# Performance work log

Hardware: AMD Instinct MI355X
Metric: run time of the kernel (lower is better)

## Reference

```python
import jax, jax.numpy as jnp
import numpy as np

N_FFT = 2048
STRIDE = 512
PAD = N_FFT // 2  # center padding removed at the end
B = 4
T = 512  # number of spectrogram frames


def _make_kernels():
    n = np.arange(N_FFT)
    # ang[out_sample, freq_bin] = 2*pi*n*k/N  (create_fourier_kernels, freq_scale='no', freq_bins=n_fft)
    ang = 2.0 * np.pi * np.outer(n, n) / N_FFT
    kernel_cos = np.cos(ang).astype(np.float32)
    kernel_sin = np.sin(ang).astype(np.float32)
    # scipy.signal.get_window('hann', N, fftbins=True) -> periodic hann
    window = (0.5 - 0.5 * np.cos(2.0 * np.pi * n / N_FFT)).astype(np.float32)
    return kernel_cos, kernel_sin, window


def setup_inputs() -> dict:
    key = jax.random.key(0)
    X = jax.random.normal(key, (B, N_FFT, T, 2), dtype=jnp.float32)
    kc, ks, w = _make_kernels()
    return {
        "X": X,
        "kernel_cos": jnp.asarray(kc),
        "kernel_sin": jnp.asarray(ks),
        "window": jnp.asarray(w),
    }


def reference(X, kernel_cos, kernel_sin, window):
    # X: (B, n_fft, T, 2) complex spectrogram (onesided=False)
    b, n_fft, t, _ = X.shape
    Xr = X[..., 0]
    Xi = X[..., 1]
    # inverse DFT via dense matmul against sinusoidal kernels (conv2d in torch):
    # frames[b, n, t] = sum_f Xr[b,f,t]*cos(2pi n f/N) - Xi[b,f,t]*sin(2pi n f/N)
    frames = (jnp.einsum('bft,nf->bnt', Xr, kernel_cos)
              - jnp.einsum('bft,nf->bnt', Xi, kernel_sin))
    frames = frames * window[None, :, None] / n_fft
    # overlap-add (torch fold): out[b, t*stride + n] += frames[b, n, t]
    out_len = n_fft + STRIDE * (t - 1)
    idx = (jnp.arange(n_fft)[:, None] + STRIDE * jnp.arange(t)[None, :]).reshape(-1)
    y = jnp.zeros((b, out_len), frames.dtype).at[:, idx].add(frames.reshape(b, -1))
    # window sum-square normalization (torch_window_sumsquare)
    w_sq = jnp.broadcast_to((window * window)[:, None], (n_fft, t)).reshape(-1)
    w_sum = jnp.zeros((out_len,), window.dtype).at[idx].add(w_sq)
    nonzero = w_sum > 1e-10
    denom = jnp.where(nonzero, w_sum, jnp.ones_like(w_sum))
    y = jnp.where(nonzero[None, :], y / denom[None, :], y)
    # center=True, length=None -> trim pad_amount from both ends
    return y[:, PAD:-PAD]
```

## Files before the change

### kernel.cpp

```cpp
#include <hip/hip_runtime.h>

#define NFFT 2048
#define TT   512
#define BB   4
#define OUTL 261632

__device__ __forceinline__ int T4(int i, int sp) {
    return ((i >> 1) << 2) | ((2 * (i & 1) + sp + (i >> 1) + (i >> 3)) & 3);
}

__device__ __forceinline__ float2 cmul(float2 a, float2 w) {
    return make_float2(a.x * w.x - a.y * w.y, a.x * w.y + a.y * w.x);
}

__device__ __forceinline__ void dft8(const float2 a[8], float2 o[8]) {
    float e0r = a[0].x + a[4].x, e0i = a[0].y + a[4].y;
    float e1r = a[0].x - a[4].x, e1i = a[0].y - a[4].y;
    float e2r = a[2].x + a[6].x, e2i = a[2].y + a[6].y;
    float e3r = a[6].y - a[2].y, e3i = a[2].x - a[6].x;
    float E0r = e0r + e2r, E0i = e0i + e2i;
    float E1r = e1r + e3r, E1i = e1i + e3i;
    float E2r = e0r - e2r, E2i = e0i - e2i;
    float E3r = e1r - e3r, E3i = e1i - e3i;
    float f0r = a[1].x + a[5].x, f0i = a[1].y + a[5].y;
    float f1r = a[1].x - a[5].x, f1i = a[1].y - a[5].y;
    float f2r = a[3].x + a[7].x, f2i = a[3].y + a[7].y;
    float f3r = a[7].y - a[3].y, f3i = a[3].x - a[7].x;
    float O0r = f0r + f2r, O0i = f0i + f2i;
    float O1r = f1r + f3r, O1i = f1i + f3i;
    float O2r = f0r - f2r, O2i = f0i - f2i;
    float O3r = f1r - f3r, O3i = f1i - f3i;
    const float h = 0.70710678118654752f;
    float W1r = h * (O1r - O1i), W1i = h * (O1r + O1i);
    float W2r = -O2i,            W2i = O2r;
    float W3r = -h * (O3r + O3i), W3i = h * (O3r - O3i);
    o[0] = make_float2(E0r + O0r, E0i + O0i);
    o[1] = make_float2(E1r + W1r, E1i + W1i);
    o[2] = make_float2(E2r + W2r, E2i + W2i);
    o[3] = make_float2(E3r + W3r, E3i + W3i);
    o[4] = make_float2(E0r - O0r, E0i - O0i);
    o[5] = make_float2(E1r - W1r, E1i - W1i);
    o[6] = make_float2(E2r - W2r, E2i - W2i);
    o[7] = make_float2(E3r - W3r, E3i - W3i);
}

__device__ __forceinline__ void twpow8(float2 o[8], float2 w1) {
    float2 w2 = cmul(w1, w1);
    float2 w3 = cmul(w2, w1);
    float2 w4 = cmul(w2, w2);
    o[1] = cmul(o[1], w1);
    o[2] = cmul(o[2], w2);
    o[3] = cmul(o[3], w3);
    o[4] = cmul(o[4], w4);
    o[5] = cmul(o[5], cmul(w4, w1));
    o[6] = cmul(o[6], cmul(w4, w2));
    o[7] = cmul(o[7], cmul(w4, w3));
}

__global__ __launch_bounds__(512, 4) void istft_k(const float* __restrict__ X,
                                                  const float* __restrict__ kc,
                                                  const float* __restrict__ ks,
                                                  const float* __restrict__ win,
                                                  float* __restrict__ out) {
    __shared__ float4 tile[4096];
    __shared__ float2 tw[256];

    const int S  = blockIdx.x;
    const int L  = ((S & 7) << 6) | (S >> 3);
    const int c0 = L * 4;
    const int b  = c0 >> 9;
    const int t0 = c0 & 511;
    const int tid = threadIdx.x;

    if (tid < 256)
        tw[tid] = make_float2(kc[2048 + tid], ks[2048 + tid]);

    const float* Xb = X + ((size_t)b * 2048 * 512 + t0) * 2;
    #pragma unroll
    for (int m = 0; m < 8; m++) {
        int f  = m * 256 + (tid >> 1);
        int sp = tid & 1;
        float4 v = *reinterpret_cast<const float4*>(Xb + (size_t)f * 1024 + sp * 4);
        tile[T4(f, sp)] = v;
    }
    __syncthreads();

    const int g = tid >> 8;
    const int u = tid & 255;

    float4 a4[8];
    float2 x0[8], x1[8], o0[8], o1[8];

    #pragma unroll
    for (int l = 0; l < 8; l++) a4[l] = tile[T4(u + 256 * l, g)];
    __syncthreads();
    #pragma unroll
    for (int l = 0; l < 8; l++) {
        x0[l] = make_float2(a4[l].x, a4[l].y);
        x1[l] = make_float2(a4[l].z, a4[l].w);
    }
    dft8(x0, o0); twpow8(o0, tw[u]);
    dft8(x1, o1); twpow8(o1, tw[u]);
    #pragma unroll
    for (int k = 0; k < 8; k++)
        tile[T4(8 * u + k, g)] = make_float4(o0[k].x, o0[k].y, o1[k].x, o1[k].y);
    __syncthreads();

    #pragma unroll
    for (int l = 0; l < 8; l++) a4[l] = tile[T4(u + 256 * l, g)];
    __syncthreads();
    #pragma unroll
    for (int l = 0; l < 8; l++) {
        x0[l] = make_float2(a4[l].x, a4[l].y);
        x1[l] = make_float2(a4[l].z, a4[l].w);
    }
    dft8(x0, o0); twpow8(o0, tw[u & ~7]);
    dft8(x1, o1); twpow8(o1, tw[u & ~7]);
    {
        int base = 64 * (u >> 3) + (u & 7);
        #pragma unroll
        for (int k = 0; k < 8; k++)
            tile[T4(base + 8 * k, g)] = make_float4(o0[k].x, o0[k].y, o1[k].x, o1[k].y);
    }
    __syncthreads();

    #pragma unroll
    for (int l = 0; l < 8; l++) a4[l] = tile[T4(u + 256 * l, g)];
    __syncthreads();
    #pragma unroll
    for (int l = 0; l < 8; l++) {
        x0[l] = make_float2(a4[l].x, a4[l].y);
        x1[l] = make_float2(a4[l].z, a4[l].w);
    }
    dft8(x0, o0); twpow8(o0, tw[u & ~63]);
    dft8(x1, o1); twpow8(o1, tw[u & ~63]);
    {
        int base = 512 * (u >> 6) + (u & 63);
        #pragma unroll
        for (int k = 0; k < 8; k++)
            tile[T4(base + 64 * k, g)] = make_float4(o0[k].x, o0[k].y, o1[k].x, o1[k].y);
    }
    __syncthreads();

    #pragma unroll
    for (int half = 0; half < 2; half++) {
        int uu = u + 256 * half;
        float4 d0 = tile[T4(uu, g)];
        float4 d1 = tile[T4(uu + 512, g)];
        float4 d2 = tile[T4(uu + 1024, g)];
        float4 d3 = tile[T4(uu + 1536, g)];
        float p0 = d0.x + d2.x, p1 = d0.x - d2.x;
        float p2 = d1.x + d3.x, p3 = d3.y - d1.y;
        float q0 = d0.z + d2.z, q1 = d0.z - d2.z;
        float q2 = d1.z + d3.z, q3 = d3.w - d1.w;
        float w0 = win[uu], w1 = win[uu + 512], w2 = win[uu + 1024], w3 = win[uu + 1536];
        tile[T4(uu, g)]        = make_float4((p0 + p2) * w0, 0.f, (q0 + q2) * w0, 0.f);
        tile[T4(uu + 512, g)]  = make_float4((p1 + p3) * w1, 0.f, (q1 + q3) * w1, 0.f);
        tile[T4(uu + 1024, g)] = make_float4((p0 - p2) * w2, 0.f, (q0 - q2) * w2, 0.f);
        tile[T4(uu + 1536, g)] = make_float4((p1 - p3) * w3, 0.f, (q1 - q3) * w3, 0.f);
    }
    __syncthreads();

    const float* tf = (const float*)tile;
    #pragma unroll 1
    for (int q = 0; q < 7; q++) {
        int jl = tid + 512 * q;
        int tb_l = jl >> 9;
        int rr = jl & 511;
        int tglob = t0 + tb_l;
        float sum = 0.f, ws = 0.f;
        #pragma unroll
        for (int k = 0; k < 4; k++) {
            int t = tglob - k;
            int n = rr + (k << 9);
            if (t >= 0 && t < TT) {
                float w = win[n];
                ws += w * w;
                int m = tb_l - k;
                if (m >= 0 && m < 4)
                    sum += tf[T4(n, m >> 1) * 4 + (m & 1) * 2];
            }
        }
        float y = sum * (1.0f / 2048.0f);
        if (ws > 1e-10f) y /= ws;
        int jp = t0 * 512 + jl - 1024;
        if (jp >= 0 && jp < OUTL) {
            float* dst = out + (size_t)b * OUTL + jp;
            if (jl >= 1536 && jl < 2048) *dst = y;
            else                         atomicAdd(dst, y);
        }
    }
}

extern "C" void kernel_launch(void* const* d_in, const int* in_sizes, int n_in,
                              void* d_out, int out_size, void* d_ws, size_t ws_size,
                              hipStream_t stream) {
    const float* X  = (const float*)d_in[0];
    const float* kc = (const float*)d_in[1];
    const float* ks = (const float*)d_in[2];
    const float* w  = (const float*)d_in[3];
    float* out = (float*)d_out;

    hipMemsetAsync(out, 0, (size_t)out_size * sizeof(float), stream);
    istft_k<<<dim3(BB * TT / 4), dim3(512), 0, stream>>>(X, kc, ks, w, out);
}
```

Before: 29.15 us.

## Shrink ISTFT blocks to two frames with register-resident FFT stages and XOR swizzle

Each block now handles 2 frames with 128 threads instead of 4 frames with 512 threads, doubling the grid. Global loads now feed the first radix-8 stage directly from registers, which drops the initial LDS staging pass. Twiddles are held in registers instead of shared memory, and the T4 layout is replaced by a simpler XOR swizzle. Interior blocks get a precomputed reciprocal of the window sum. Every output element is now written with atomicAdd, so there are more atomics in exchange for less shared memory per block and higher occupancy.

```diff
diff --git a/kernel.cpp b/kernel.cpp
--- a/kernel.cpp
+++ b/kernel.cpp
@@ -1,13 +1,10 @@
 #include <hip/hip_runtime.h>
 
-#define NFFT 2048
 #define TT   512
 #define BB   4
 #define OUTL 261632
 
-__device__ __forceinline__ int T4(int i, int sp) {
-    return ((i >> 1) << 2) | ((2 * (i & 1) + sp + (i >> 1) + (i >> 3)) & 3);
-}
+__device__ __forceinline__ int sw(int x) { return x ^ ((x >> 3) & 7); }
 
 __device__ __forceinline__ float2 cmul(float2 a, float2 w) {
     return make_float2(a.x * w.x - a.y * w.y, a.x * w.y + a.y * w.x);
@@ -57,138 +54,171 @@
     o[7] = cmul(o[7], cmul(w4, w3));
 }
 
-__global__ __launch_bounds__(512, 4) void istft_k(const float* __restrict__ X,
-                                                  const float* __restrict__ kc,
-                                                  const float* __restrict__ ks,
-                                                  const float* __restrict__ win,
-                                                  float* __restrict__ out) {
-    __shared__ float4 tile[4096];
-    __shared__ float2 tw[256];
+__device__ __forceinline__ void bfly8(const float4 a[8], float2 w1,
+                                      float4* tile, int base8) {
+    float2 x0[8], x1[8], o0[8], o1[8];
+    #pragma unroll
+    for (int l = 0; l < 8; l++) {
+        x0[l] = make_float2(a[l].x, a[l].y);
+        x1[l] = make_float2(a[l].z, a[l].w);
+    }
+    dft8(x0, o0); twpow8(o0, w1);
+    dft8(x1, o1); twpow8(o1, w1);
+    #pragma unroll
+    for (int k = 0; k < 8; k++)
+        tile[sw(base8 + k)] = make_float4(o0[k].x, o0[k].y, o1[k].x, o1[k].y);
+}
+
+__global__ __launch_bounds__(128) void istft_k(const float* __restrict__ X,
+                                               const float* __restrict__ kc,
+                                               const float* __restrict__ ks,
+                                               const float* __restrict__ win,
+                                               float* __restrict__ out) {
+    __shared__ float4 tile[2048];
 
     const int S  = blockIdx.x;
-    const int L  = ((S & 7) << 6) | (S >> 3);
-    const int c0 = L * 4;
+    const int L  = ((S & 7) << 7) | (S >> 3);
+    const int c0 = L * 2;
     const int b  = c0 >> 9;
     const int t0 = c0 & 511;
-    const int tid = threadIdx.x;
-
-    if (tid < 256)
-        tw[tid] = make_float2(kc[2048 + tid], ks[2048 + tid]);
+    const int u  = threadIdx.x;
+
+    const float* twc = kc + 2048;
+    const float* tws = ks + 2048;
+
+    const int mB = 8 * (u >> 3), mC = 64 * (u >> 6);
+    float2 wA0 = make_float2(twc[u], tws[u]);
+    float2 wA1 = make_float2(twc[u + 128], tws[u + 128]);
+    float2 wB0 = make_float2(twc[mB], tws[mB]);
+    float2 wB1 = make_float2(twc[mB + 128], tws[mB + 128]);
+    float2 wC0 = make_float2(twc[mC], tws[mC]);
+    float2 wC1 = make_float2(twc[mC + 128], tws[mC + 128]);
 
     const float* Xb = X + ((size_t)b * 2048 * 512 + t0) * 2;
-    #pragma unroll
-    for (int m = 0; m < 8; m++) {
-        int f  = m * 256 + (tid >> 1);
-        int sp = tid & 1;
-        float4 v = *reinterpret_cast<const float4*>(Xb + (size_t)f * 1024 + sp * 4);
-        tile[T4(f, sp)] = v;
-    }
-    __syncthreads();
-
-    const int g = tid >> 8;
-    const int u = tid & 255;
-
-    float4 a4[8];
-    float2 x0[8], x1[8], o0[8], o1[8];
-
-    #pragma unroll
-    for (int l = 0; l < 8; l++) a4[l] = tile[T4(u + 256 * l, g)];
-    __syncthreads();
-    #pragma unroll
-    for (int l = 0; l < 8; l++) {
-        x0[l] = make_float2(a4[l].x, a4[l].y);
-        x1[l] = make_float2(a4[l].z, a4[l].w);
-    }
-    dft8(x0, o0); twpow8(o0, tw[u]);
-    dft8(x1, o1); twpow8(o1, tw[u]);
-    #pragma unroll
-    for (int k = 0; k < 8; k++)
-        tile[T4(8 * u + k, g)] = make_float4(o0[k].x, o0[k].y, o1[k].x, o1[k].y);
-    __syncthreads();
-
-    #pragma unroll
-    for (int l = 0; l < 8; l++) a4[l] = tile[T4(u + 256 * l, g)];
-    __syncthreads();
-    #pragma unroll
-    for (int l = 0; l < 8; l++) {
-        x0[l] = make_float2(a4[l].x, a4[l].y);
-        x1[l] = make_float2(a4[l].z, a4[l].w);
-    }
-    dft8(x0, o0); twpow8(o0, tw[u & ~7]);
-    dft8(x1, o1); twpow8(o1, tw[u & ~7]);
+    float4 a0[8], a1[8];
+    #pragma unroll
+    for (int l = 0; l < 8; l++) {
+        a0[l] = *reinterpret_cast<const float4*>(Xb + (size_t)(u + 256 * l) * 1024);
+        a1[l] = *reinterpret_cast<const float4*>(Xb + (size_t)(u + 128 + 256 * l) * 1024);
+    }
+    bfly8(a0, wA0, tile, 8 * u);
+    bfly8(a1, wA1, tile, 8 * (u + 128));
+    __syncthreads();
+
+    #pragma unroll
+    for (int l = 0; l < 8; l++) {
+        a0[l] = tile[sw(u + 256 * l)];
+        a1[l] = tile[sw(u + 128 + 256 * l)];
+    }
+    __syncthreads();
     {
-        int base = 64 * (u >> 3) + (u & 7);
-        #pragma unroll
-        for (int k = 0; k < 8; k++)
-            tile[T4(base + 8 * k, g)] = make_float4(o0[k].x, o0[k].y, o1[k].x, o1[k].y);
-    }
-    __syncthreads();
-
-    #pragma unroll
-    for (int l = 0; l < 8; l++) a4[l] = tile[T4(u + 256 * l, g)];
-    __syncthreads();
-    #pragma unroll
-    for (int l = 0; l < 8; l++) {
-        x0[l] = make_float2(a4[l].x, a4[l].y);
-        x1[l] = make_float2(a4[l].z, a4[l].w);
-    }
-    dft8(x0, o0); twpow8(o0, tw[u & ~63]);
-    dft8(x1, o1); twpow8(o1, tw[u & ~63]);
+        int b0 = 64 * (u >> 3) + (u & 7);
+        float2 x0[8], x1[8], o0[8], o1[8];
+        #pragma unroll
+        for (int l = 0; l < 8; l++) { x0[l] = make_float2(a0[l].x, a0[l].y); x1[l] = make_float2(a0[l].z, a0[l].w); }
+        dft8(x0, o0); twpow8(o0, wB0);
+        dft8(x1, o1); twpow8(o1, wB0);
+        #pragma unroll
+        for (int k = 0; k < 8; k++)
+            tile[sw(b0 + 8 * k)] = make_float4(o0[k].x, o0[k].y, o1[k].x, o1[k].y);
+        #pragma unroll
+        for (int l = 0; l < 8; l++) { x0[l] = make_float2(a1[l].x, a1[l].y); x1[l] = make_float2(a1[l].z, a1[l].w); }
+        dft8(x0, o0); twpow8(o0, wB1);
+        dft8(x1, o1); twpow8(o1, wB1);
+        #pragma unroll
+        for (int k = 0; k < 8; k++)
+            tile[sw(b0 + 1024 + 8 * k)] = make_float4(o0[k].x, o0[k].y, o1[k].x, o1[k].y);
+    }
+    __syncthreads();
+
+    #pragma unroll
+    for (int l = 0; l < 8; l++) {
+        a0[l] = tile[sw(u + 256 * l)];
+        a1[l] = tile[sw(u + 128 + 256 * l)];
+    }
+    __syncthreads();
     {
-        int base = 512 * (u >> 6) + (u & 63);
-        #pragma unroll
-        for (int k = 0; k < 8; k++)
-            tile[T4(base + 64 * k, g)] = make_float4(o0[k].x, o0[k].y, o1[k].x, o1[k].y);
-    }
-    __syncthreads();
-
-    #pragma unroll
-    for (int half = 0; half < 2; half++) {
-        int uu = u + 256 * half;
-        float4 d0 = tile[T4(uu, g)];
-        float4 d1 = tile[T4(uu + 512, g)];
-        float4 d2 = tile[T4(uu + 1024, g)];
-        float4 d3 = tile[T4(uu + 1536, g)];
+        int b0 = 512 * (u >> 6) + (u & 63);
+        float2 x0[8], x1[8], o0[8], o1[8];
+        #pragma unroll
+        for (int l = 0; l < 8; l++) { x0[l] = make_float2(a0[l].x, a0[l].y); x1[l] = make_float2(a0[l].z, a0[l].w); }
+        dft8(x0, o0); twpow8(o0, wC0);
+        dft8(x1, o1); twpow8(o1, wC0);
+        #pragma unroll
+        for (int k = 0; k < 8; k++)
+            tile[sw(b0 + 64 * k)] = make_float4(o0[k].x, o0[k].y, o1[k].x, o1[k].y);
+        #pragma unroll
+        for (int l = 0; l < 8; l++) { x0[l] = make_float2(a1[l].x, a1[l].y); x1[l] = make_float2(a1[l].z, a1[l].w); }
+        dft8(x0, o0); twpow8(o0, wC1);
+        dft8(x1, o1); twpow8(o1, wC1);
+        #pragma unroll
+        for (int k = 0; k < 8; k++)
+            tile[sw(b0 + 1024 + 64 * k)] = make_float4(o0[k].x, o0[k].y, o1[k].x, o1[k].y);
+    }
+    __syncthreads();
+
+    float4 d[4][4];
+    #pragma unroll
+    for (int bi = 0; bi < 4; bi++) {
+        int j = u + 128 * bi;
+        #pragma unroll
+        for (int m = 0; m < 4; m++) d[bi][m] = tile[sw(j + 512 * m)];
+    }
+    __syncthreads();
+    float2* fD = (float2*)tile;
+    #pragma unroll
+    for (int bi = 0; bi < 4; bi++) {
+        int j = u + 128 * bi;
+        float4 d0 = d[bi][0], d1 = d[bi][1], d2 = d[bi][2], d3 = d[bi][3];
         float p0 = d0.x + d2.x, p1 = d0.x - d2.x;
         float p2 = d1.x + d3.x, p3 = d3.y - d1.y;
         float q0 = d0.z + d2.z, q1 = d0.z - d2.z;
         float q2 = d1.z + d3.z, q3 = d3.w - d1.w;
-        float w0 = win[uu], w1 = win[uu + 512], w2 = win[uu + 1024], w3 = win[uu + 1536];
-        tile[T4(uu, g)]        = make_float4((p0 + p2) * w0, 0.f, (q0 + q2) * w0, 0.f);
-        tile[T4(uu + 512, g)]  = make_float4((p1 + p3) * w1, 0.f, (q1 + q3) * w1, 0.f);
-        tile[T4(uu + 1024, g)] = make_float4((p0 - p2) * w2, 0.f, (q0 - q2) * w2, 0.f);
-        tile[T4(uu + 1536, g)] = make_float4((p1 - p3) * w3, 0.f, (q1 - q3) * w3, 0.f);
-    }
-    __syncthreads();
-
-    const float* tf = (const float*)tile;
+        float w0 = win[j], w1 = win[j + 512], w2 = win[j + 1024], w3 = win[j + 1536];
+        fD[j]        = make_float2((p0 + p2) * w0, (q0 + q2) * w0);
+        fD[j + 512]  = make_float2((p1 + p3) * w1, (q1 + q3) * w1);
+        fD[j + 1024] = make_float2((p0 - p2) * w2, (q0 - q2) * w2);
+        fD[j + 1536] = make_float2((p1 - p3) * w3, (q1 - q3) * w3);
+    }
+    __syncthreads();
+
+    const bool interior = (t0 >= 3) && (t0 <= 507);
+    float invw[4];
+    if (interior) {
+        #pragma unroll
+        for (int i = 0; i < 4; i++) {
+            int rr = u + 128 * i;
+            float s = 0.f;
+            #pragma unroll
+            for (int k = 0; k < 4; k++) { float w = win[rr + 512 * k]; s += w * w; }
+            invw[i] = 1.0f / (2048.0f * s);
+        }
+    }
+    float* outb = out + (size_t)b * OUTL;
     #pragma unroll 1
-    for (int q = 0; q < 7; q++) {
-        int jl = tid + 512 * q;
-        int tb_l = jl >> 9;
-        int rr = jl & 511;
-        int tglob = t0 + tb_l;
-        float sum = 0.f, ws = 0.f;
-        #pragma unroll
-        for (int k = 0; k < 4; k++) {
-            int t = tglob - k;
-            int n = rr + (k << 9);
-            if (t >= 0 && t < TT) {
-                float w = win[n];
-                ws += w * w;
-                int m = tb_l - k;
-                if (m >= 0 && m < 4)
-                    sum += tf[T4(n, m >> 1) * 4 + (m & 1) * 2];
+    for (int q = 0; q < 20; q++) {
+        int jl = u + 128 * q;
+        float contrib = 0.f;
+        if (jl < 2048) contrib += fD[jl].x;
+        if (jl >= 512) contrib += fD[jl - 512].y;
+        int j  = t0 * 512 + jl;
+        int jp = j - 1024;
+        if (jp < 0 || jp >= OUTL) continue;
+        float y;
+        if (interior) {
+            y = contrib * invw[q & 3];
+        } else {
+            int tb = j >> 9, r = j & 511;
+            float s = 0.f;
+            #pragma unroll
+            for (int k = 0; k < 4; k++) {
+                int t = tb - k;
+                if (t >= 0 && t < TT) { float w = win[r + (k << 9)]; s += w * w; }
             }
+            y = contrib * (1.0f / 2048.0f);
+            if (s > 1e-10f) y /= s;
         }
-        float y = sum * (1.0f / 2048.0f);
-        if (ws > 1e-10f) y /= ws;
-        int jp = t0 * 512 + jl - 1024;
-        if (jp >= 0 && jp < OUTL) {
-            float* dst = out + (size_t)b * OUTL + jp;
-            if (jl >= 1536 && jl < 2048) *dst = y;
-            else                         atomicAdd(dst, y);
-        }
+        atomicAdd(outb + jp, y);
     }
 }
 
@@ -202,5 +232,5 @@
     float* out = (float*)d_out;
 
     hipMemsetAsync(out, 0, (size_t)out_size * sizeof(float), stream);
-    istft_k<<<dim3(BB * TT / 4), dim3(512), 0, stream>>>(X, kc, ks, w, out);
-}
+    istft_k<<<dim3(BB * TT / 2), dim3(128), 0, stream>>>(X, kc, ks, w, out);
+}
```

Result: slower. 40.73 us (+39.7%).
